# Optimization experiments

Measured on AMD Instinct MI355X. Metric: run time of the kernel, lower is better.

## Reference

```python
import jax, jax.numpy as jnp
import numpy as np

NQ = 20
P_MAX = 480 * 640 - 1  # hardcoded clamp in original module


def make_quantizer_params(nq=NQ, mn=0.0, mx=1.0):
    # Replicates APLoss.__init__ conv1d weight/bias initialization.
    a = (nq - 1) / (mx - mn)
    w = np.concatenate([-a * np.ones(nq), a * np.ones(nq)]).astype(np.float32)
    b = np.concatenate([a * mn + np.arange(nq, 0, -1),
                        np.arange(2 - nq, 2, 1) - a * mn]).astype(np.float32)
    w[0] = w[-1] = 0.0
    b[0] = b[-1] = 1.0
    return jnp.asarray(w), jnp.asarray(b)


def setup_inputs() -> dict:
    key = jax.random.key(0)
    k1, k2, k3, k4, k5 = jax.random.split(key, 5)
    P, D, N, NEG = 307200, 64, 20000, 80
    qw, qb = make_quantizer_params()
    return {
        "descriptors1": jax.random.normal(k1, (1, P, D), dtype=jnp.float32),
        "descriptors2": jax.random.normal(k2, (1, P, D), dtype=jnp.float32),
        "qw": qw,
        "qb": qb,
        "matches_1": jax.random.randint(k3, (N,), 0, P),
        "matches_2": jax.random.randint(k4, (N,), 0, P),
        "offsets": jax.random.randint(k5, (NEG,), 0, 640),
    }


def reference(descriptors1, descriptors2, qw, qb, matches_1, matches_2, offsets):
    nq = qw.shape[0] // 2
    d1 = descriptors1[0]  # (P, D)
    d2 = descriptors2[0]  # (P, D)

    # negative indices: offset positive matches, clamp to valid pixel range
    non_m2 = jnp.clip(matches_2[:, None] + offsets[None, :], 0, P_MAX)  # (N, NEG)

    a1 = d1[matches_1]                                  # (N, D)
    pos = jnp.sum(a1 * d2[matches_2], axis=-1)          # (N,)
    neg = jnp.einsum('nd,nmd->nm', a1, d2[non_m2])      # (N, NEG)

    scores = jnp.concatenate([pos[:, None], neg], axis=1)   # (N, M), M = 1+NEG
    label = jnp.zeros_like(scores).at[:, 0].set(1.0)         # (N, M)

    # soft quantizer: 1x1 conv == per-bin affine; min of two halves, relu
    x = scores[:, None, :]                                   # (N, 1, M)
    q = jnp.minimum(qw[:nq, None] * x + qb[:nq, None],
                    qw[nq:, None] * x + qb[nq:, None])
    q = jnp.maximum(q, 0.0)                                  # (N, nq, M)

    nbs = q.sum(axis=-1)                                     # (N, nq)
    rec = (q * label[:, None, :]).sum(axis=-1)               # (N, nq)
    prec = jnp.cumsum(rec, axis=-1) / (1e-16 + jnp.cumsum(nbs, axis=-1))
    rec = rec / rec.sum(axis=-1, keepdims=True)
    ap = (prec * rec).sum(axis=-1)                           # (N,)
    return (1.0 - ap).mean()
```

## Files before the change

### kernel.cpp

```cpp
#include <hip/hip_runtime.h>

#define DIM 64


__global__ __launch_bounds__(256) void k_zero(int* __restrict__ cnt, int nbuck) {
    int i = blockIdx.x * 256 + threadIdx.x;
    if (i < nbuck) cnt[i] = 0;
}

__global__ __launch_bounds__(256) void k_hist(const int* __restrict__ m2,
                                              int* __restrict__ cnt, int N) {
    int n = blockIdx.x * 256 + threadIdx.x;
    if (n < N) atomicAdd(&cnt[m2[n] >> 7], 1);
}

__global__ __launch_bounds__(256) void k_scan(int* __restrict__ cnt, int nbuck) {
    __shared__ int s[256];
    const int tid = threadIdx.x;
    const int base = tid * 10;
    int loc[10];
    int sum = 0;
    #pragma unroll
    for (int i = 0; i < 10; ++i) {
        int idx = base + i;
        int v = (idx < nbuck) ? cnt[idx] : 0;
        loc[i] = sum;
        sum += v;
    }
    s[tid] = sum;
    __syncthreads();
    for (int off = 1; off < 256; off <<= 1) {
        int v = (tid >= off) ? s[tid - off] : 0;
        __syncthreads();
        s[tid] += v;
        __syncthreads();
    }
    const int excl = (tid > 0) ? s[tid - 1] : 0;
    #pragma unroll
    for (int i = 0; i < 10; ++i) {
        int idx = base + i;
        if (idx < nbuck) cnt[idx] = excl + loc[i];
    }
}

__global__ __launch_bounds__(256) void k_scatter(const int* __restrict__ m2,
                                                 int* __restrict__ cnt,
                                                 int* __restrict__ perm, int N) {
    int n = blockIdx.x * 256 + threadIdx.x;
    if (n < N) {
        int pos = atomicAdd(&cnt[m2[n] >> 7], 1);
        perm[pos] = n;
    }
}


__global__ __launch_bounds__(256) void pixel_ap_main(
    const float* __restrict__ d1, const float* __restrict__ d2,
    const float* __restrict__ qw, const float* __restrict__ qb,
    const int* __restrict__ m1, const int* __restrict__ m2,
    const int* __restrict__ offs, const int* __restrict__ perm,
    float* __restrict__ partial, int P, int NEG, int NQ2)
{
    const int tid = threadIdx.x;
    const int nq  = NQ2 >> 1;
    const int M   = NEG + 1;

    __shared__ float s_a1[DIM];
    __shared__ int   s_off[128];
    __shared__ float s_scores[160];
    __shared__ float s_red[8];

    const int n  = perm[blockIdx.x];
    const int i1 = m1[n];
    const int i2 = m2[n];

    if (tid < DIM) s_a1[tid] = d1[(size_t)i1 * DIM + tid];
    if (tid >= 64 && tid < 64 + NEG) s_off[tid - 64] = offs[tid - 64];
    __syncthreads();

    const int g = tid >> 4;
    const int l = tid & 15;
    const float4 a4 = ((const float4*)s_a1)[l];

    float4 bv[6];
    #pragma unroll
    for (int t = 0; t < 6; ++t) {
        const int j = g + 16 * t;
        if (j < M) {
            const int row = (j == 0) ? i2 : min(i2 + s_off[j - 1], P - 1);
            bv[t] = ((const float4*)(d2 + (size_t)row * DIM))[l];
        }
    }
    #pragma unroll
    for (int t = 0; t < 6; ++t) {
        const int j = g + 16 * t;
        if (j < M) {
            float s = bv[t].x * a4.x + bv[t].y * a4.y + bv[t].z * a4.z + bv[t].w * a4.w;
            s += __shfl_xor(s, 1);
            s += __shfl_xor(s, 2);
            s += __shfl_xor(s, 4);
            s += __shfl_xor(s, 8);
            if (l == 0) s_scores[j] = s;
        }
    }
    __syncthreads();

    const float a_scale = qw[nq];
    const float amn     = qb[nq - 1] - 1.0f;
    const float ulim    = (float)(nq - 1);

    const float xp = s_scores[0];
    const float up = fminf(fmaxf(a_scale * xp - amn, 0.0f), ulim);
    const float ip = floorf(up);
    const float fp = up - ip;

    float n1 = 0.0f, n2 = 0.0f;
    if (tid < M) {
        const float x = s_scores[tid];
        const float u = fminf(fmaxf(a_scale * x - amn, 0.0f), ulim);
        const float fi = floorf(u);
        const float f  = u - fi;
        n2 = (fi >= ip)        ? 1.0f : ((fi == ip - 1.0f) ? f : 0.0f);
        n1 = (fi >= ip + 1.0f) ? 1.0f : ((fi == ip)        ? f : 0.0f);
    }
    #pragma unroll
    for (int off = 32; off >= 1; off >>= 1) {
        n1 += __shfl_down(n1, off);
        n2 += __shfl_down(n2, off);
    }
    const int wid = tid >> 6;
    if ((tid & 63) == 0) { s_red[wid] = n1; s_red[4 + wid] = n2; }
    __syncthreads();
    if (tid == 0) {
        const float N1 = s_red[0] + s_red[1] + s_red[2] + s_red[3];
        const float N2 = s_red[4] + s_red[5] + s_red[6] + s_red[7];
        const float ap = fp * fp / (1e-16f + N1) + (1.0f - fp) / (1e-16f + N2);
        partial[n] = 1.0f - ap;
    }
}


__global__ __launch_bounds__(256) void k_reduce1(const float* __restrict__ partial,
                                                 float* __restrict__ partial2, int N) {
    float s = 0.0f;
    for (int i = blockIdx.x * 256 + threadIdx.x; i < N; i += gridDim.x * 256) s += partial[i];
    #pragma unroll
    for (int off = 32; off >= 1; off >>= 1) s += __shfl_down(s, off);
    __shared__ float s_w[4];
    if ((threadIdx.x & 63) == 0) s_w[threadIdx.x >> 6] = s;
    __syncthreads();
    if (threadIdx.x == 0) partial2[blockIdx.x] = s_w[0] + s_w[1] + s_w[2] + s_w[3];
}

__global__ __launch_bounds__(64) void k_reduce2(const float* __restrict__ partial2,
                                                float* __restrict__ out, int nb, int N) {
    float s = 0.0f;
    for (int i = threadIdx.x; i < nb; i += 64) s += partial2[i];
    #pragma unroll
    for (int off = 32; off >= 1; off >>= 1) s += __shfl_down(s, off);
    if (threadIdx.x == 0) out[0] = s / (float)N;
}

extern "C" void kernel_launch(void* const* d_in, const int* in_sizes, int n_in,
                              void* d_out, int out_size, void* d_ws, size_t ws_size,
                              hipStream_t stream) {
    const float* d1   = (const float*)d_in[0];
    const float* d2   = (const float*)d_in[1];
    const float* qw   = (const float*)d_in[2];
    const float* qb   = (const float*)d_in[3];
    const int*   m1   = (const int*)d_in[4];
    const int*   m2   = (const int*)d_in[5];
    const int*   offs = (const int*)d_in[6];

    const int N    = in_sizes[4];
    const int P    = in_sizes[0] / DIM;
    const int NEG  = in_sizes[6];
    const int NQ2  = in_sizes[2];
    const int nbuck = (P + 127) >> 7;

    int*   cnt      = (int*)d_ws;
    int*   perm     = cnt + nbuck;
    float* partial  = (float*)(perm + N);
    float* partial2 = partial + N;
    const int RB = 80;

    const int nblk = (N + 255) / 256;

    k_zero   <<<(nbuck + 255) / 256, 256, 0, stream>>>(cnt, nbuck);
    k_hist   <<<nblk, 256, 0, stream>>>(m2, cnt, N);
    k_scan   <<<1, 256, 0, stream>>>(cnt, nbuck);
    k_scatter<<<nblk, 256, 0, stream>>>(m2, cnt, perm, N);

    pixel_ap_main<<<N, 256, 0, stream>>>(d1, d2, qw, qb, m1, m2, offs, perm,
                                         partial, P, NEG, NQ2);

    k_reduce1<<<RB, 256, 0, stream>>>(partial, partial2, N);
    k_reduce2<<<1, 64, 0, stream>>>(partial2, (float*)d_out, RB, N);
}
```

Before: 203.7 us.

## Process one match per wave, fuse sort kernels, and merge reductions

Result: slower. 222.2 us (+9.1%).

```diff
diff --git a/kernel.cpp b/kernel.cpp
--- a/kernel.cpp
+++ b/kernel.cpp
@@ -1,106 +1,106 @@
 #include <hip/hip_runtime.h>
 
 #define DIM 64
+#define MAXBUCK 2560
+#define SORT_T 1024
 
+__global__ __launch_bounds__(1024) void k_sort(const int* __restrict__ m2,
+                                               int* __restrict__ perm, int N, int nbuck)
+{
+    __shared__ int cnt[MAXBUCK];
+    __shared__ int s[SORT_T];
+    const int tid = threadIdx.x;
 
-__global__ __launch_bounds__(256) void k_zero(int* __restrict__ cnt, int nbuck) {
-    int i = blockIdx.x * 256 + threadIdx.x;
-    if (i < nbuck) cnt[i] = 0;
-}
+    for (int i = tid; i < nbuck; i += SORT_T) cnt[i] = 0;
+    __syncthreads();
+    for (int i = tid; i < N; i += SORT_T) atomicAdd(&cnt[m2[i] >> 7], 1);
+    __syncthreads();
 
-__global__ __launch_bounds__(256) void k_hist(const int* __restrict__ m2,
-                                              int* __restrict__ cnt, int N) {
-    int n = blockIdx.x * 256 + threadIdx.x;
-    if (n < N) atomicAdd(&cnt[m2[n] >> 7], 1);
-}
-
-__global__ __launch_bounds__(256) void k_scan(int* __restrict__ cnt, int nbuck) {
-    __shared__ int s[256];
-    const int tid = threadIdx.x;
-    const int base = tid * 10;
-    int loc[10];
+    const int base = tid * 3;
+    int loc[3];
     int sum = 0;
     #pragma unroll
-    for (int i = 0; i < 10; ++i) {
-        int idx = base + i;
-        int v = (idx < nbuck) ? cnt[idx] : 0;
-        loc[i] = sum;
+    for (int u = 0; u < 3; ++u) {
+        const int idx = base + u;
+        const int v = (idx < nbuck) ? cnt[idx] : 0;
+        loc[u] = sum;
         sum += v;
     }
     s[tid] = sum;
     __syncthreads();
-    for (int off = 1; off < 256; off <<= 1) {
-        int v = (tid >= off) ? s[tid - off] : 0;
+    for (int off = 1; off < SORT_T; off <<= 1) {
+        const int v = (tid >= off) ? s[tid - off] : 0;
         __syncthreads();
         s[tid] += v;
         __syncthreads();
     }
     const int excl = (tid > 0) ? s[tid - 1] : 0;
     #pragma unroll
-    for (int i = 0; i < 10; ++i) {
-        int idx = base + i;
-        if (idx < nbuck) cnt[idx] = excl + loc[i];
+    for (int u = 0; u < 3; ++u) {
+        const int idx = base + u;
+        if (idx < nbuck) cnt[idx] = excl + loc[u];
+    }
+    __syncthreads();
+    for (int i = tid; i < N; i += SORT_T) {
+        const int pos = atomicAdd(&cnt[m2[i] >> 7], 1);
+        perm[pos] = i;
     }
 }
-
-__global__ __launch_bounds__(256) void k_scatter(const int* __restrict__ m2,
-                                                 int* __restrict__ cnt,
-                                                 int* __restrict__ perm, int N) {
-    int n = blockIdx.x * 256 + threadIdx.x;
-    if (n < N) {
-        int pos = atomicAdd(&cnt[m2[n] >> 7], 1);
-        perm[pos] = n;
-    }
-}
-
 
 __global__ __launch_bounds__(256) void pixel_ap_main(
     const float* __restrict__ d1, const float* __restrict__ d2,
     const float* __restrict__ qw, const float* __restrict__ qb,
     const int* __restrict__ m1, const int* __restrict__ m2,
     const int* __restrict__ offs, const int* __restrict__ perm,
-    float* __restrict__ partial, int P, int NEG, int NQ2)
+    float* __restrict__ partial, int P, int NEG, int NQ2, int N)
 {
-    const int tid = threadIdx.x;
-    const int nq  = NQ2 >> 1;
-    const int M   = NEG + 1;
+    const int tid  = threadIdx.x;
+    const int wave = tid >> 6;
+    const int lane = tid & 63;
+    const int nq   = NQ2 >> 1;
+    const int M    = NEG + 1;
 
-    __shared__ float s_a1[DIM];
     __shared__ int   s_off[128];
-    __shared__ float s_scores[160];
-    __shared__ float s_red[8];
+    __shared__ float s_scores[4][96];
 
-    const int n  = perm[blockIdx.x];
+    if (tid < NEG) s_off[tid] = offs[tid];
+    __syncthreads();
+
+    const int b    = blockIdx.x;
+    const int per  = (gridDim.x + 7) >> 3;
+    const int pos  = (b & 7) * per + (b >> 3);
+    const int sid0 = pos * 4 + wave;
+    const int sid  = min(sid0, N - 1);
+
+    const int n  = perm[sid];
     const int i1 = m1[n];
     const int i2 = m2[n];
 
-    if (tid < DIM) s_a1[tid] = d1[(size_t)i1 * DIM + tid];
-    if (tid >= 64 && tid < 64 + NEG) s_off[tid - 64] = offs[tid - 64];
-    __syncthreads();
+    const int g = lane >> 4;
+    const int l = lane & 15;
+    const float4 a4 = ((const float4*)(d1 + (size_t)i1 * DIM))[l];
 
-    const int g = tid >> 4;
-    const int l = tid & 15;
-    const float4 a4 = ((const float4*)s_a1)[l];
-
-    float4 bv[6];
-    #pragma unroll
-    for (int t = 0; t < 6; ++t) {
-        const int j = g + 16 * t;
-        if (j < M) {
-            const int row = (j == 0) ? i2 : min(i2 + s_off[j - 1], P - 1);
-            bv[t] = ((const float4*)(d2 + (size_t)row * DIM))[l];
+    for (int c = 0; c < 3; ++c) {
+        float4 bv[7];
+        #pragma unroll
+        for (int u = 0; u < 7; ++u) {
+            const int j = g + 4 * (7 * c + u);
+            if (j < M) {
+                const int row = (j == 0) ? i2 : min(i2 + s_off[j - 1], P - 1);
+                bv[u] = ((const float4*)(d2 + (size_t)row * DIM))[l];
+            }
         }
-    }
-    #pragma unroll
-    for (int t = 0; t < 6; ++t) {
-        const int j = g + 16 * t;
-        if (j < M) {
-            float s = bv[t].x * a4.x + bv[t].y * a4.y + bv[t].z * a4.z + bv[t].w * a4.w;
-            s += __shfl_xor(s, 1);
-            s += __shfl_xor(s, 2);
-            s += __shfl_xor(s, 4);
-            s += __shfl_xor(s, 8);
-            if (l == 0) s_scores[j] = s;
+        #pragma unroll
+        for (int u = 0; u < 7; ++u) {
+            const int j = g + 4 * (7 * c + u);
+            if (j < M) {
+                float sd = bv[u].x * a4.x + bv[u].y * a4.y + bv[u].z * a4.z + bv[u].w * a4.w;
+                sd += __shfl_xor(sd, 1);
+                sd += __shfl_xor(sd, 2);
+                sd += __shfl_xor(sd, 4);
+                sd += __shfl_xor(sd, 8);
+                if (l == 0) s_scores[wave][j] = sd;
+            }
         }
     }
     __syncthreads();
@@ -109,56 +109,56 @@
     const float amn     = qb[nq - 1] - 1.0f;
     const float ulim    = (float)(nq - 1);
 
-    const float xp = s_scores[0];
+    const float xp = s_scores[wave][0];
     const float up = fminf(fmaxf(a_scale * xp - amn, 0.0f), ulim);
     const float ip = floorf(up);
     const float fp = up - ip;
 
     float n1 = 0.0f, n2 = 0.0f;
-    if (tid < M) {
-        const float x = s_scores[tid];
-        const float u = fminf(fmaxf(a_scale * x - amn, 0.0f), ulim);
+    if (lane < M) {
+        const float x  = s_scores[wave][lane];
+        const float u  = fminf(fmaxf(a_scale * x - amn, 0.0f), ulim);
         const float fi = floorf(u);
         const float f  = u - fi;
-        n2 = (fi >= ip)        ? 1.0f : ((fi == ip - 1.0f) ? f : 0.0f);
-        n1 = (fi >= ip + 1.0f) ? 1.0f : ((fi == ip)        ? f : 0.0f);
+        n2 += (fi >= ip)        ? 1.0f : ((fi == ip - 1.0f) ? f : 0.0f);
+        n1 += (fi >= ip + 1.0f) ? 1.0f : ((fi == ip)        ? f : 0.0f);
+    }
+    const int j2 = lane + 64;
+    if (j2 < M) {
+        const float x  = s_scores[wave][j2];
+        const float u  = fminf(fmaxf(a_scale * x - amn, 0.0f), ulim);
+        const float fi = floorf(u);
+        const float f  = u - fi;
+        n2 += (fi >= ip)        ? 1.0f : ((fi == ip - 1.0f) ? f : 0.0f);
+        n1 += (fi >= ip + 1.0f) ? 1.0f : ((fi == ip)        ? f : 0.0f);
     }
     #pragma unroll
     for (int off = 32; off >= 1; off >>= 1) {
-        n1 += __shfl_down(n1, off);
-        n2 += __shfl_down(n2, off);
+        n1 += __shfl_xor(n1, off);
+        n2 += __shfl_xor(n2, off);
     }
-    const int wid = tid >> 6;
-    if ((tid & 63) == 0) { s_red[wid] = n1; s_red[4 + wid] = n2; }
-    __syncthreads();
-    if (tid == 0) {
-        const float N1 = s_red[0] + s_red[1] + s_red[2] + s_red[3];
-        const float N2 = s_red[4] + s_red[5] + s_red[6] + s_red[7];
-        const float ap = fp * fp / (1e-16f + N1) + (1.0f - fp) / (1e-16f + N2);
+    if (lane == 0 && sid0 < N) {
+        const float ap = fp * fp / (1e-16f + n1) + (1.0f - fp) / (1e-16f + n2);
         partial[n] = 1.0f - ap;
     }
 }
 
-
-__global__ __launch_bounds__(256) void k_reduce1(const float* __restrict__ partial,
-                                                 float* __restrict__ partial2, int N) {
+__global__ __launch_bounds__(1024) void k_reduce(const float* __restrict__ partial,
+                                                 float* __restrict__ out, int N)
+{
     float s = 0.0f;
-    for (int i = blockIdx.x * 256 + threadIdx.x; i < N; i += gridDim.x * 256) s += partial[i];
+    for (int i = threadIdx.x; i < N; i += 1024) s += partial[i];
     #pragma unroll
-    for (int off = 32; off >= 1; off >>= 1) s += __shfl_down(s, off);
-    __shared__ float s_w[4];
-    if ((threadIdx.x & 63) == 0) s_w[threadIdx.x >> 6] = s;
+    for (int off = 32; off >= 1; off >>= 1) s += __shfl_xor(s, off);
+    __shared__ float sw[16];
+    if ((threadIdx.x & 63) == 0) sw[threadIdx.x >> 6] = s;
     __syncthreads();
-    if (threadIdx.x == 0) partial2[blockIdx.x] = s_w[0] + s_w[1] + s_w[2] + s_w[3];
-}
-
-__global__ __launch_bounds__(64) void k_reduce2(const float* __restrict__ partial2,
-                                                float* __restrict__ out, int nb, int N) {
-    float s = 0.0f;
-    for (int i = threadIdx.x; i < nb; i += 64) s += partial2[i];
-    #pragma unroll
-    for (int off = 32; off >= 1; off >>= 1) s += __shfl_down(s, off);
-    if (threadIdx.x == 0) out[0] = s / (float)N;
+    if (threadIdx.x == 0) {
+        float t = 0.0f;
+        #pragma unroll
+        for (int w = 0; w < 16; ++w) t += sw[w];
+        out[0] = t / (float)N;
+    }
 }
 
 extern "C" void kernel_launch(void* const* d_in, const int* in_sizes, int n_in,
@@ -172,28 +172,20 @@
     const int*   m2   = (const int*)d_in[5];
     const int*   offs = (const int*)d_in[6];
 
-    const int N    = in_sizes[4];
-    const int P    = in_sizes[0] / DIM;
-    const int NEG  = in_sizes[6];
-    const int NQ2  = in_sizes[2];
+    const int N     = in_sizes[4];
+    const int P     = in_sizes[0] / DIM;
+    const int NEG   = in_sizes[6];
+    const int NQ2   = in_sizes[2];
     const int nbuck = (P + 127) >> 7;
 
-    int*   cnt      = (int*)d_ws;
-    int*   perm     = cnt + nbuck;
-    float* partial  = (float*)(perm + N);
-    float* partial2 = partial + N;
-    const int RB = 80;
+    int*   perm    = (int*)d_ws;
+    float* partial = (float*)(perm + N);
 
-    const int nblk = (N + 255) / 256;
+    k_sort<<<1, SORT_T, 0, stream>>>(m2, perm, N, nbuck);
 
-    k_zero   <<<(nbuck + 255) / 256, 256, 0, stream>>>(cnt, nbuck);
-    k_hist   <<<nblk, 256, 0, stream>>>(m2, cnt, N);
-    k_scan   <<<1, 256, 0, stream>>>(cnt, nbuck);
-    k_scatter<<<nblk, 256, 0, stream>>>(m2, cnt, perm, N);
+    const int nb = (N + 3) / 4;
+    pixel_ap_main<<<nb, 256, 0, stream>>>(d1, d2, qw, qb, m1, m2, offs, perm,
+                                          partial, P, NEG, NQ2, N);
 
-    pixel_ap_main<<<N, 256, 0, stream>>>(d1, d2, qw, qb, m1, m2, offs, perm,
-                                         partial, P, NEG, NQ2);
-
-    k_reduce1<<<RB, 256, 0, stream>>>(partial, partial2, N);
-    k_reduce2<<<1, 64, 0, stream>>>(partial2, (float*)d_out, RB, N);
+    k_reduce<<<1, 1024, 0, stream>>>(partial, (float*)d_out, N);
 }
```
